# Kernel tuning notes

Measured on AMD Instinct MI355X. Metric: run time of the kernel, lower is better.

The kernel has to match this reference:

```python
import jax, jax.numpy as jnp
import numpy as np

N_NODES = 100000


def setup_inputs() -> dict:
    key = jax.random.key(0)
    k1, k2, k3, k4, k5 = jax.random.split(key, 5)
    x = jax.random.normal(k1, (N_NODES, 256), dtype=jnp.float32)
    edge_index = jax.random.randint(k2, (2, 3200000), 0, N_NODES, dtype=jnp.int64)
    edge_weight = jax.random.uniform(k3, (3200000,), dtype=jnp.float32)
    W = jax.random.normal(k4, (256, 128), dtype=jnp.float32) / np.sqrt(256.0)
    b = jax.random.normal(k5, (128,), dtype=jnp.float32) * 0.01
    return {"x": x, "edge_index": edge_index, "edge_weight": edge_weight, "W": W, "b": b}


def reference(x, edge_index, edge_weight, W, b):
    # Dense linear projection: h = x @ W + b  -> [N, out_feats]
    h = x @ W + b
    # SpMM aggregation: out[dst] += w_e * h[src]
    src = edge_index[1]  # column indices (neighbors)
    dst = edge_index[0]  # row indices (output nodes)
    msgs = h[src] * edge_weight[:, None]  # [E, out_feats]
    out = jax.ops.segment_sum(msgs, dst, num_segments=x.shape[0])
    return out
```

## Files before the change

### kernel.cpp

```cpp
#include <hip/hip_runtime.h>

#define K_IN   256
#define N_OUT  128
#define BM     32
#define SCAN_CHUNK 1024
#define NBLK   512
#define BSHIFT 7
#define BNODES 128
#define CAP    8192

typedef short bf16x8 __attribute__((ext_vector_type(8)));
typedef float f32x4  __attribute__((ext_vector_type(4)));

static __device__ __forceinline__ unsigned short f2bf(float f) {
    unsigned u = __float_as_uint(f);
    unsigned r = (u + 0x7FFF + ((u >> 16) & 1)) >> 16;
    return (unsigned short)r;
}
static __device__ __forceinline__ float bf2f(unsigned short b) {
    return __uint_as_float(((unsigned)b) << 16);
}

__global__ __launch_bounds__(256) void prep_w(const float* __restrict__ W, char* __restrict__ wbt)
{
    const int t = blockIdx.x * 256 + threadIdx.x;
    if (t >= N_OUT * 32) return;
    const int n = t >> 5;
    const int c = t & 31;
    unsigned v[4];
#pragma unroll
    for (int p = 0; p < 4; ++p) {
        const unsigned lo = f2bf(W[(size_t)(c * 8 + 2 * p)     * N_OUT + n]);
        const unsigned hi = f2bf(W[(size_t)(c * 8 + 2 * p + 1) * N_OUT + n]);
        v[p] = lo | (hi << 16);
    }
    const int byte = n * 512 + ((c * 16) ^ ((n & 7) << 4));
    *reinterpret_cast<uint4*>(wbt + byte) = make_uint4(v[0], v[1], v[2], v[3]);
}

__global__ __launch_bounds__(256) void gcn_gemm(
    const float* __restrict__ x, const uint4* __restrict__ wbt,
    const float* __restrict__ bias, unsigned short* __restrict__ hb, int M)
{
    __shared__ uint4 smem4[81920 / 16];
    char* smem = (char*)smem4;
    const int tid  = threadIdx.x;
    const int row0 = blockIdx.x * BM;

    {
        uint4* wl = (uint4*)smem;
#pragma unroll
        for (int it = 0; it < 16; ++it) wl[it * 256 + tid] = wbt[it * 256 + tid];
    }
    {
        const int r    = tid >> 3;
        const int ks   = tid & 7;
        const int grow = row0 + r;
        char* xbase    = smem + 65536 + r * 512;
        const int swz  = (r & 7) << 4;
        if (grow < M) {
            const float4* src = reinterpret_cast<const float4*>(x + (size_t)grow * K_IN + ks * 32);
#pragma unroll
            for (int q = 0; q < 8; ++q) {
                const float4 f = src[q];
                uint2 v;
                v.x = (unsigned)f2bf(f.x) | ((unsigned)f2bf(f.y) << 16);
                v.y = (unsigned)f2bf(f.z) | ((unsigned)f2bf(f.w) << 16);
                const int kb = ks * 64 + q * 8;
                *reinterpret_cast<uint2*>(xbase + (((kb & ~15) ^ swz) | (kb & 15))) = v;
            }
        } else {
            const uint2 z = make_uint2(0u, 0u);
#pragma unroll
            for (int q = 0; q < 8; ++q) {
                const int kb = ks * 64 + q * 8;
                *reinterpret_cast<uint2*>(xbase + (((kb & ~15) ^ swz) | (kb & 15))) = z;
            }
        }
    }
    __syncthreads();

    const int lane = tid & 63;
    const int wv   = tid >> 6;
    const int wr   = wv >> 1;
    const int wc   = wv & 1;
    const int l15  = lane & 15;
    const int lk   = lane >> 4;

    const int  arow = wr * 16 + l15;
    const char* xrow = smem + 65536 + arow * 512;
    const int  aswz = (arow & 7) << 4;
    const int  bswz = (l15 & 7) << 4;
    const char* brow0 = smem + (size_t)(wc * 64 + l15) * 512;

    f32x4 acc[4] = {};

#pragma unroll
    for (int ks = 0; ks < 8; ++ks) {
        const int kb = ks * 64 + lk * 16;
        const bf16x8 a = *reinterpret_cast<const bf16x8*>(xrow + (kb ^ aswz));
        const int bk = kb ^ bswz;
#pragma unroll
        for (int j = 0; j < 4; ++j) {
            const bf16x8 b = *reinterpret_cast<const bf16x8*>(brow0 + j * (16 * 512) + bk);
            acc[j] = __builtin_amdgcn_mfma_f32_16x16x32_bf16(a, b, acc[j], 0, 0, 0);
        }
    }

#pragma unroll
    for (int j = 0; j < 4; ++j) {
        const int gcol = wc * 64 + j * 16 + l15;
        const float bv = bias[gcol];
#pragma unroll
        for (int r = 0; r < 4; ++r) {
            const int grow = row0 + wr * 16 + lk * 4 + r;
            if (grow < M)
                hb[(size_t)grow * N_OUT + gcol] = f2bf(acc[j][r] + bv);
        }
    }
}

__global__ __launch_bounds__(256) void hist_buckets(
    const int* __restrict__ ei, int E, int M, int B, int* __restrict__ histG, int chunk)
{
    __shared__ int h[1024];
    for (int i = threadIdx.x; i < B; i += 256) h[i] = 0;
    __syncthreads();
    const int beg = blockIdx.x * chunk;
    const int end = min(beg + chunk, E);
    for (int i = beg + threadIdx.x; i < end; i += 256) {
        const int d = ei[i];
        const int s = ei[(size_t)E + i];
        if ((unsigned)d < (unsigned)M && (unsigned)s < (unsigned)M)
            atomicAdd(&h[d >> BSHIFT], 1);
    }
    __syncthreads();
    for (int i = threadIdx.x; i < B; i += 256) histG[i * NBLK + blockIdx.x] = h[i];
}

__global__ __launch_bounds__(256) void scan_block_sums(
    const int* __restrict__ cnt, int n, int* __restrict__ bsum)
{
    __shared__ int sd[256];
    const int base = blockIdx.x * SCAN_CHUNK + threadIdx.x * 4;
    int s = 0;
#pragma unroll
    for (int j = 0; j < 4; ++j) { const int idx = base + j; if (idx < n) s += cnt[idx]; }
    sd[threadIdx.x] = s; __syncthreads();
    for (int off = 128; off > 0; off >>= 1) {
        if (threadIdx.x < off) sd[threadIdx.x] += sd[threadIdx.x + off];
        __syncthreads();
    }
    if (threadIdx.x == 0) bsum[blockIdx.x] = sd[0];
}

__global__ __launch_bounds__(1024) void scan_sums(
    int* __restrict__ bsum, int nb, int* __restrict__ P, int n)
{
    __shared__ int sd[1024];
    const int t = threadIdx.x;
    const int v = (t < nb) ? bsum[t] : 0;
    sd[t] = v; __syncthreads();
    for (int off = 1; off < 1024; off <<= 1) {
        const int add = (t >= off) ? sd[t - off] : 0;
        __syncthreads();
        sd[t] += add;
        __syncthreads();
    }
    if (t < nb) bsum[t] = sd[t] - v;
    if (t == nb - 1) P[n] = sd[t];
}

__global__ __launch_bounds__(256) void scan_write_offsets(
    const int* __restrict__ cnt, int n, const int* __restrict__ bsum, int* __restrict__ P)
{
    __shared__ int sd[256];
    const int t = threadIdx.x;
    const int base = blockIdx.x * SCAN_CHUNK + t * 4;
    int v[4]; int s = 0;
#pragma unroll
    for (int j = 0; j < 4; ++j) { const int idx = base + j; v[j] = (idx < n) ? cnt[idx] : 0; s += v[j]; }
    sd[t] = s; __syncthreads();
    const int own = s;
    for (int off = 1; off < 256; off <<= 1) {
        const int add = (t >= off) ? sd[t - off] : 0;
        __syncthreads();
        sd[t] += add;
        __syncthreads();
    }
    int run = bsum[blockIdx.x] + (sd[t] - own);
#pragma unroll
    for (int j = 0; j < 4; ++j) {
        const int idx = base + j;
        if (idx < n) { P[idx] = run; run += v[j]; }
    }
}

__global__ __launch_bounds__(256) void scatter_records(
    const int* __restrict__ ei, const float* __restrict__ ew, int E, int M, int B,
    const int* __restrict__ P, uint2* __restrict__ rec, int chunk)
{
    __shared__ int cur[1024];
    for (int i = threadIdx.x; i < B; i += 256) cur[i] = P[i * NBLK + blockIdx.x];
    __syncthreads();
    const int beg = blockIdx.x * chunk;
    const int end = min(beg + chunk, E);
    for (int i = beg + threadIdx.x; i < end; i += 256) {
        const int d = ei[i];
        const int s = ei[(size_t)E + i];
        if ((unsigned)d >= (unsigned)M || (unsigned)s >= (unsigned)M) continue;
        const int pos = atomicAdd(&cur[d >> BSHIFT], 1);
        rec[pos] = make_uint2((unsigned)s | ((unsigned)(d & (BNODES - 1)) << 24),
                              __float_as_uint(ew[i]));
    }
}

__global__ __launch_bounds__(256) void sort_bucket(
    const int* __restrict__ P, uint2* __restrict__ rec,
    int* __restrict__ offsN, int* __restrict__ bflag, int M, int B)
{
    __shared__ uint2 srt[CAP];
    __shared__ int hist[BNODES];
    __shared__ int tmp[BNODES];
    __shared__ int cur[BNODES];

    const int b   = blockIdx.x;
    const int tid = threadIdx.x;
    const int beg = P[b * NBLK];
    const int end = P[(b + 1) * NBLK];
    const int cnt = end - beg;
    const int node0 = b << BSHIFT;

    if (tid < BNODES) hist[tid] = 0;
    if (tid == 0) bflag[b] = (cnt <= CAP) ? 0 : 1;
    if (tid == 0 && b == B - 1) offsN[M] = end;
    __syncthreads();

    if (cnt > CAP) {
        if (tid < BNODES) {
            const int node = node0 + tid;
            if (node < M) offsN[node] = beg;
        }
        return;
    }

    for (int i = beg + tid; i < end; i += 256) {
        const uint2 r = rec[i];
        srt[i - beg] = r;
        atomicAdd(&hist[r.x >> 24], 1);
    }
    __syncthreads();
    if (tid < BNODES) tmp[tid] = hist[tid];
    __syncthreads();
    for (int off = 1; off < BNODES; off <<= 1) {
        int v = 0;
        if (tid < BNODES && tid >= off) v = tmp[tid - off];
        __syncthreads();
        if (tid < BNODES) tmp[tid] += v;
        __syncthreads();
    }
    if (tid < BNODES) {
        const int excl = tmp[tid] - hist[tid];
        cur[tid] = excl;
        const int node = node0 + tid;
        if (node < M) offsN[node] = beg + excl;
    }
    __syncthreads();

    for (int i = tid; i < cnt; i += 256) {
        const uint2 r = srt[i];
        const int pos = atomicAdd(&cur[r.x >> 24], 1);
        rec[beg + pos] = r;
    }
}

__global__ __launch_bounds__(256) void gather_kernel(
    const int* __restrict__ offsN, const int* __restrict__ P,
    const int* __restrict__ bflag, const uint2* __restrict__ rec,
    const unsigned short* __restrict__ hb, float* __restrict__ out, int M)
{
    const int n = blockIdx.x * 4 + (threadIdx.x >> 6);
    if (n >= M) return;
    const int lane = threadIdx.x & 63;
    const int b = n >> BSHIFT;

    float ax = 0.f, ay = 0.f;

    if (bflag[b] == 0) {
        const int beg = offsN[n], end = offsN[n + 1];
        int i = beg;
        for (; i + 4 <= end; i += 4) {
            const uint2 r0 = rec[i],     r1 = rec[i + 1];
            const uint2 r2 = rec[i + 2], r3 = rec[i + 3];
            const float w0 = __uint_as_float(r0.y), w1 = __uint_as_float(r1.y);
            const float w2 = __uint_as_float(r2.y), w3 = __uint_as_float(r3.y);
            const unsigned u0 = reinterpret_cast<const unsigned*>(hb + (size_t)(r0.x & 0xFFFFFF) * N_OUT)[lane];
            const unsigned u1 = reinterpret_cast<const unsigned*>(hb + (size_t)(r1.x & 0xFFFFFF) * N_OUT)[lane];
            const unsigned u2 = reinterpret_cast<const unsigned*>(hb + (size_t)(r2.x & 0xFFFFFF) * N_OUT)[lane];
            const unsigned u3 = reinterpret_cast<const unsigned*>(hb + (size_t)(r3.x & 0xFFFFFF) * N_OUT)[lane];
            ax += w0 * bf2f((unsigned short)u0) + w1 * bf2f((unsigned short)u1)
                + w2 * bf2f((unsigned short)u2) + w3 * bf2f((unsigned short)u3);
            ay += w0 * bf2f((unsigned short)(u0 >> 16)) + w1 * bf2f((unsigned short)(u1 >> 16))
                + w2 * bf2f((unsigned short)(u2 >> 16)) + w3 * bf2f((unsigned short)(u3 >> 16));
        }
        for (; i < end; ++i) {
            const uint2 r = rec[i];
            const float w = __uint_as_float(r.y);
            const unsigned u = reinterpret_cast<const unsigned*>(hb + (size_t)(r.x & 0xFFFFFF) * N_OUT)[lane];
            ax += w * bf2f((unsigned short)u);
            ay += w * bf2f((unsigned short)(u >> 16));
        }
    } else {
        const int beg = P[b * NBLK], end = P[(b + 1) * NBLK];
        const unsigned want = (unsigned)(n & (BNODES - 1));
        for (int i = beg; i < end; ++i) {
            const uint2 r = rec[i];
            if ((r.x >> 24) != want) continue;
            const float w = __uint_as_float(r.y);
            const unsigned u = reinterpret_cast<const unsigned*>(hb + (size_t)(r.x & 0xFFFFFF) * N_OUT)[lane];
            ax += w * bf2f((unsigned short)u);
            ay += w * bf2f((unsigned short)(u >> 16));
        }
    }

    reinterpret_cast<float2*>(out + (size_t)n * N_OUT)[lane] = make_float2(ax, ay);
}

extern "C" void kernel_launch(void* const* d_in, const int* in_sizes, int n_in,
                              void* d_out, int out_size, void* d_ws, size_t ws_size,
                              hipStream_t stream)
{
    const float* x    = (const float*)d_in[0];
    const int*   ei   = (const int*)d_in[1];
    const float* ew   = (const float*)d_in[2];
    const float* W    = (const float*)d_in[3];
    const float* bias = (const float*)d_in[4];
    float* out = (float*)d_out;

    const int M = in_sizes[0] / K_IN;
    const int E = in_sizes[1] / 2;
    const int B = (M + BNODES - 1) >> BSHIFT;
    const int n = B * NBLK;
    const int nb = (n + SCAN_CHUNK - 1) / SCAN_CHUNK;
    const int chunk = (E + NBLK - 1) / NBLK;

    auto align256 = [](size_t v) { return (v + 255) & ~(size_t)255; };
    const size_t o_hb    = 0;
    const size_t o_hist  = align256(o_hb + (size_t)M * N_OUT * sizeof(unsigned short));
    const size_t o_P     = align256(o_hist + (size_t)n * sizeof(int));
    const size_t o_bsum  = align256(o_P + (size_t)(n + 1) * sizeof(int));
    const size_t o_offsN = align256(o_bsum + (size_t)1024 * sizeof(int));
    const size_t o_bflag = align256(o_offsN + (size_t)(M + 1) * sizeof(int));
    const size_t o_wbt   = align256(o_bflag + (size_t)B * sizeof(int));
    const size_t o_rec   = align256(o_wbt + (size_t)65536);

    unsigned short* hb    = (unsigned short*)((char*)d_ws + o_hb);
    int*            histG = (int*)((char*)d_ws + o_hist);
    int*            P     = (int*)((char*)d_ws + o_P);
    int*            bsum  = (int*)((char*)d_ws + o_bsum);
    int*            offsN = (int*)((char*)d_ws + o_offsN);
    int*            bflag = (int*)((char*)d_ws + o_bflag);
    char*           wbt   = (char*)d_ws + o_wbt;
    uint2*          rec   = (uint2*)((char*)d_ws + o_rec);

    prep_w<<<16, 256, 0, stream>>>(W, wbt);
    gcn_gemm<<<(M + BM - 1) / BM, 256, 0, stream>>>(x, (const uint4*)wbt, bias, hb, M);
    hist_buckets<<<NBLK, 256, 0, stream>>>(ei, E, M, B, histG, chunk);
    scan_block_sums<<<nb, 256, 0, stream>>>(histG, n, bsum);
    scan_sums<<<1, 1024, 0, stream>>>(bsum, nb, P, n);
    scan_write_offsets<<<nb, 256, 0, stream>>>(histG, n, bsum, P);
    scatter_records<<<NBLK, 256, 0, stream>>>(ei, ew, E, M, B, P, rec, chunk);
    sort_bucket<<<B, 256, 0, stream>>>(P, rec, offsN, bflag, M, B);
    gather_kernel<<<(M + 3) / 4, 256, 0, stream>>>(offsN, P, bflag, rec, hb, out, M);
}
```

Baseline: 265.6 us.

## Fuse bucket histogram into GEMM, sub-sort by source, deepen gather unroll

The destination-bucket histogram moves into the tail of the GEMM kernel's first NBLK blocks, which saves one kernel launch and lets the histogram overlap with GEMM work. The histogram pass no longer reads source indices, and the node-range bounds checks are removed from both the histogram and scatter. The per-bucket sort now keys on local destination plus the high bits of the source (2048 keys), so each node's neighbours are ordered by source for better cache locality in the gather. The gather loop is unrolled to 8 edges to keep more loads in flight. Dropping the bounds checks assumes every edge index is valid.

Measured after the change: 266.9 us. About the same (+0.5%).

```diff
diff --git a/kernel.cpp b/kernel.cpp
--- a/kernel.cpp
+++ b/kernel.cpp
@@ -8,6 +8,7 @@
 #define BSHIFT 7
 #define BNODES 128
 #define CAP    8192
+#define NKEY   2048
 
 typedef short bf16x8 __attribute__((ext_vector_type(8)));
 typedef float f32x4  __attribute__((ext_vector_type(4)));
@@ -40,7 +41,9 @@
 
 __global__ __launch_bounds__(256) void gcn_gemm(
     const float* __restrict__ x, const uint4* __restrict__ wbt,
-    const float* __restrict__ bias, unsigned short* __restrict__ hb, int M)
+    const float* __restrict__ bias, unsigned short* __restrict__ hb,
+    const int* __restrict__ ei, int* __restrict__ histG,
+    int M, int E, int B, int chunk)
 {
     __shared__ uint4 smem4[81920 / 16];
     char* smem = (char*)smem4;
@@ -118,24 +121,19 @@
                 hb[(size_t)grow * N_OUT + gcol] = f2bf(acc[j][r] + bv);
         }
     }
-}
-
-__global__ __launch_bounds__(256) void hist_buckets(
-    const int* __restrict__ ei, int E, int M, int B, int* __restrict__ histG, int chunk)
-{
-    __shared__ int h[1024];
-    for (int i = threadIdx.x; i < B; i += 256) h[i] = 0;
-    __syncthreads();
-    const int beg = blockIdx.x * chunk;
-    const int end = min(beg + chunk, E);
-    for (int i = beg + threadIdx.x; i < end; i += 256) {
-        const int d = ei[i];
-        const int s = ei[(size_t)E + i];
-        if ((unsigned)d < (unsigned)M && (unsigned)s < (unsigned)M)
-            atomicAdd(&h[d >> BSHIFT], 1);
-    }
-    __syncthreads();
-    for (int i = threadIdx.x; i < B; i += 256) histG[i * NBLK + blockIdx.x] = h[i];
+
+    if (blockIdx.x < NBLK) {
+        __syncthreads();
+        int* bins = (int*)smem;
+        for (int i = tid; i < B; i += 256) bins[i] = 0;
+        __syncthreads();
+        const int beg = blockIdx.x * chunk;
+        const int end = min(beg + chunk, E);
+        for (int i = beg + tid; i < end; i += 256)
+            atomicAdd(&bins[ei[i] >> BSHIFT], 1);
+        __syncthreads();
+        for (int i = tid; i < B; i += 256) histG[i * NBLK + blockIdx.x] = bins[i];
+    }
 }
 
 __global__ __launch_bounds__(256) void scan_block_sums(
@@ -208,7 +206,6 @@
     for (int i = beg + threadIdx.x; i < end; i += 256) {
         const int d = ei[i];
         const int s = ei[(size_t)E + i];
-        if ((unsigned)d >= (unsigned)M || (unsigned)s >= (unsigned)M) continue;
         const int pos = atomicAdd(&cur[d >> BSHIFT], 1);
         rec[pos] = make_uint2((unsigned)s | ((unsigned)(d & (BNODES - 1)) << 24),
                               __float_as_uint(ew[i]));
@@ -220,9 +217,8 @@
     int* __restrict__ offsN, int* __restrict__ bflag, int M, int B)
 {
     __shared__ uint2 srt[CAP];
-    __shared__ int hist[BNODES];
-    __shared__ int tmp[BNODES];
-    __shared__ int cur[BNODES];
+    __shared__ int hist[NKEY];
+    __shared__ int sd[256];
 
     const int b   = blockIdx.x;
     const int tid = threadIdx.x;
@@ -231,7 +227,7 @@
     const int cnt = end - beg;
     const int node0 = b << BSHIFT;
 
-    if (tid < BNODES) hist[tid] = 0;
+    for (int i = tid; i < NKEY; i += 256) hist[i] = 0;
     if (tid == 0) bflag[b] = (cnt <= CAP) ? 0 : 1;
     if (tid == 0 && b == B - 1) offsN[M] = end;
     __syncthreads();
@@ -247,29 +243,37 @@
     for (int i = beg + tid; i < end; i += 256) {
         const uint2 r = rec[i];
         srt[i - beg] = r;
-        atomicAdd(&hist[r.x >> 24], 1);
-    }
-    __syncthreads();
-    if (tid < BNODES) tmp[tid] = hist[tid];
-    __syncthreads();
-    for (int off = 1; off < BNODES; off <<= 1) {
-        int v = 0;
-        if (tid < BNODES && tid >= off) v = tmp[tid - off];
-        __syncthreads();
-        if (tid < BNODES) tmp[tid] += v;
-        __syncthreads();
-    }
+        const int key = ((r.x >> 24) << 4) | ((r.x & 0xFFFFFF) >> 13);
+        atomicAdd(&hist[key], 1);
+    }
+    __syncthreads();
+
+    const int base = tid * 8;
+    int v[8]; int s = 0;
+#pragma unroll
+    for (int j = 0; j < 8; ++j) { v[j] = hist[base + j]; s += v[j]; }
+    sd[tid] = s; __syncthreads();
+    for (int off = 1; off < 256; off <<= 1) {
+        const int add = (tid >= off) ? sd[tid - off] : 0;
+        __syncthreads();
+        sd[tid] += add;
+        __syncthreads();
+    }
+    int run = sd[tid] - s;
+#pragma unroll
+    for (int j = 0; j < 8; ++j) { hist[base + j] = run; run += v[j]; }
+    __syncthreads();
+
     if (tid < BNODES) {
-        const int excl = tmp[tid] - hist[tid];
-        cur[tid] = excl;
         const int node = node0 + tid;
-        if (node < M) offsN[node] = beg + excl;
+        if (node < M) offsN[node] = beg + hist[tid << 4];
     }
     __syncthreads();
 
     for (int i = tid; i < cnt; i += 256) {
         const uint2 r = srt[i];
-        const int pos = atomicAdd(&cur[r.x >> 24], 1);
+        const int key = ((r.x >> 24) << 4) | ((r.x & 0xFFFFFF) >> 13);
+        const int pos = atomicAdd(&hist[key], 1);
         rec[beg + pos] = r;
     }
 }
@@ -283,30 +287,31 @@
     if (n >= M) return;
     const int lane = threadIdx.x & 63;
     const int b = n >> BSHIFT;
+    const unsigned* __restrict__ hb32 = reinterpret_cast<const unsigned*>(hb);
 
     float ax = 0.f, ay = 0.f;
 
     if (bflag[b] == 0) {
         const int beg = offsN[n], end = offsN[n + 1];
         int i = beg;
-        for (; i + 4 <= end; i += 4) {
-            const uint2 r0 = rec[i],     r1 = rec[i + 1];
-            const uint2 r2 = rec[i + 2], r3 = rec[i + 3];
-            const float w0 = __uint_as_float(r0.y), w1 = __uint_as_float(r1.y);
-            const float w2 = __uint_as_float(r2.y), w3 = __uint_as_float(r3.y);
-            const unsigned u0 = reinterpret_cast<const unsigned*>(hb + (size_t)(r0.x & 0xFFFFFF) * N_OUT)[lane];
-            const unsigned u1 = reinterpret_cast<const unsigned*>(hb + (size_t)(r1.x & 0xFFFFFF) * N_OUT)[lane];
-            const unsigned u2 = reinterpret_cast<const unsigned*>(hb + (size_t)(r2.x & 0xFFFFFF) * N_OUT)[lane];
-            const unsigned u3 = reinterpret_cast<const unsigned*>(hb + (size_t)(r3.x & 0xFFFFFF) * N_OUT)[lane];
-            ax += w0 * bf2f((unsigned short)u0) + w1 * bf2f((unsigned short)u1)
-                + w2 * bf2f((unsigned short)u2) + w3 * bf2f((unsigned short)u3);
-            ay += w0 * bf2f((unsigned short)(u0 >> 16)) + w1 * bf2f((unsigned short)(u1 >> 16))
-                + w2 * bf2f((unsigned short)(u2 >> 16)) + w3 * bf2f((unsigned short)(u3 >> 16));
+        for (; i + 8 <= end; i += 8) {
+            unsigned u[8]; float w[8];
+#pragma unroll
+            for (int q = 0; q < 8; ++q) {
+                const uint2 r = rec[i + q];
+                w[q] = __uint_as_float(r.y);
+                u[q] = hb32[(size_t)((r.x & 0xFFFFFF) << 6) + lane];
+            }
+#pragma unroll
+            for (int q = 0; q < 8; ++q) {
+                ax += w[q] * bf2f((unsigned short)u[q]);
+                ay += w[q] * bf2f((unsigned short)(u[q] >> 16));
+            }
         }
         for (; i < end; ++i) {
             const uint2 r = rec[i];
             const float w = __uint_as_float(r.y);
-            const unsigned u = reinterpret_cast<const unsigned*>(hb + (size_t)(r.x & 0xFFFFFF) * N_OUT)[lane];
+            const unsigned u = hb32[(size_t)((r.x & 0xFFFFFF) << 6) + lane];
             ax += w * bf2f((unsigned short)u);
             ay += w * bf2f((unsigned short)(u >> 16));
         }
@@ -317,7 +322,7 @@
             const uint2 r = rec[i];
             if ((r.x >> 24) != want) continue;
             const float w = __uint_as_float(r.y);
-            const unsigned u = reinterpret_cast<const unsigned*>(hb + (size_t)(r.x & 0xFFFFFF) * N_OUT)[lane];
+            const unsigned u = hb32[(size_t)((r.x & 0xFFFFFF) << 6) + lane];
             ax += w * bf2f((unsigned short)u);
             ay += w * bf2f((unsigned short)(u >> 16));
         }
@@ -364,8 +369,8 @@
     uint2*          rec   = (uint2*)((char*)d_ws + o_rec);
 
     prep_w<<<16, 256, 0, stream>>>(W, wbt);
-    gcn_gemm<<<(M + BM - 1) / BM, 256, 0, stream>>>(x, (const uint4*)wbt, bias, hb, M);
-    hist_buckets<<<NBLK, 256, 0, stream>>>(ei, E, M, B, histG, chunk);
+    gcn_gemm<<<(M + BM - 1) / BM, 256, 0, stream>>>(
+        x, (const uint4*)wbt, bias, hb, ei, histG, M, E, B, chunk);
     scan_block_sums<<<nb, 256, 0, stream>>>(histG, n, bsum);
     scan_sums<<<1, 1024, 0, stream>>>(bsum, nb, P, n);
     scan_write_offsets<<<nb, 256, 0, stream>>>(histG, n, bsum, P);
```
